# Kernel tuning notes

Measured on AMD Instinct MI355X. Metric: run time of the kernel, lower is better.

Reference implementation:

```python
import jax, jax.numpy as jnp
import numpy as np

N_NODES = 50000
N_EDGES = 800000
NUM_FEATURES = 128
HIDDEN = 128
EMBED = 64
OUT_DIM = 1


def setup_inputs() -> dict:
    key = jax.random.key(0)
    ks = jax.random.split(key, 12)
    x = jax.random.normal(ks[0], (N_NODES, NUM_FEATURES), dtype=jnp.float32)
    edge_index = jax.random.randint(ks[1], (2, N_EDGES), 0, N_NODES, dtype=jnp.int64)

    def glorot(k, fan_in, fan_out):
        s = jnp.sqrt(6.0 / (fan_in + fan_out)).astype(jnp.float32)
        return jax.random.uniform(k, (fan_in, fan_out), jnp.float32, -s, s)

    return {
        "x": x,
        "edge_index": edge_index,
        "W1": glorot(ks[2], NUM_FEATURES, HIDDEN),
        "b1": jnp.zeros((HIDDEN,), jnp.float32),
        "Wh": glorot(ks[3], HIDDEN, HIDDEN),
        "bh": jnp.zeros((HIDDEN,), jnp.float32),
        "W2": glorot(ks[4], HIDDEN, EMBED),
        "b2": jnp.zeros((EMBED,), jnp.float32),
        "Wout": glorot(ks[5], EMBED, OUT_DIM),
        "bout": jnp.zeros((OUT_DIM,), jnp.float32),
    }


def _gcn_norm(edge_index, num_nodes):
    # Add self-loops, compute symmetric normalization deg^{-1/2} A_hat deg^{-1/2}
    loop = jnp.arange(num_nodes, dtype=edge_index.dtype)
    src = jnp.concatenate([edge_index[0], loop])
    dst = jnp.concatenate([edge_index[1], loop])
    deg = jax.ops.segment_sum(jnp.ones_like(dst, dtype=jnp.float32), dst,
                              num_segments=num_nodes)
    dis = jnp.where(deg > 0, jax.lax.rsqrt(jnp.maximum(deg, 1.0)), 0.0)
    norm = dis[src] * dis[dst]  # [E+N]
    return src, dst, norm


def _gcn_conv(h, W, b, src, dst, norm, num_nodes):
    h = h @ W  # linear transform first (PyG GCNConv)
    msg = h[src] * norm[:, None]  # gather + scale
    return jax.ops.segment_sum(msg, dst, num_segments=num_nodes) + b


def reference(x, edge_index, W1, b1, Wh, bh, W2, b2, Wout, bout):
    n = x.shape[0]
    src, dst, norm = _gcn_norm(edge_index, n)
    h = jax.nn.relu(_gcn_conv(x, W1, b1, src, dst, norm, n))  # dropout p=0 -> identity
    h = jax.nn.relu(_gcn_conv(h, Wh, bh, src, dst, norm, n))
    h = _gcn_conv(h, W2, b2, src, dst, norm, n)
    out = h @ Wout + bout
    return (out, h)
```

## Files before the change

kernel.cpp:

```cpp
#include <hip/hip_runtime.h>
#include <hip/hip_bf16.h>


#define N_NODES 50000
#define N_EDGES 800000
#define NBUCK 196
#define GB 196
#define EPB 4096

typedef __attribute__((ext_vector_type(8))) short short8;
typedef __attribute__((ext_vector_type(8))) unsigned short ushort8v;
typedef __attribute__((ext_vector_type(4))) float f32x4;

static __device__ __forceinline__ unsigned short f2bf(float f) {
    __hip_bfloat16 h = __float2bfloat16(f);
    return *reinterpret_cast<unsigned short*>(&h);
}
static __device__ __forceinline__ float bf2f(unsigned short u) {
    return __uint_as_float(((unsigned)u) << 16);
}


__global__ __launch_bounds__(256) void hist_wprep_kernel(
    const int* __restrict__ dstv, int* __restrict__ H, int nE, int* __restrict__ ticket,
    const float* __restrict__ W1, const float* __restrict__ Wh, const float* __restrict__ W2,
    unsigned short* __restrict__ W1hi, unsigned short* __restrict__ W1lo,
    unsigned short* __restrict__ Whhi, unsigned short* __restrict__ Whlo,
    unsigned short* __restrict__ W2hi, unsigned short* __restrict__ W2lo) {
    int gt = blockIdx.x * 256 + threadIdx.x;
    if (gt == 0) *ticket = 0;
    if (gt < 40960) {
        const float* W;
        unsigned short *Hi, *Lo;
        int nout, lt;
        if (gt < 16384)      { W = W1; Hi = W1hi; Lo = W1lo; nout = 128; lt = gt; }
        else if (gt < 32768) { W = Wh; Hi = Whhi; Lo = Whlo; nout = 128; lt = gt - 16384; }
        else                 { W = W2; Hi = W2hi; Lo = W2lo; nout = 64;  lt = gt - 32768; }
        int col = lt % nout, k = lt / nout;
        float v = W[lt];
        unsigned short hi = f2bf(v);
        unsigned short lo = f2bf(v - bf2f(hi));
        Hi[(size_t)col * 128 + k] = hi;
        Lo[(size_t)col * 128 + k] = lo;
    }

    __shared__ int h[NBUCK];
    for (int i = threadIdx.x; i < NBUCK; i += 256) h[i] = 0;
    __syncthreads();
    int base = blockIdx.x * EPB;
#pragma unroll
    for (int i = 0; i < EPB / 256; ++i) {
        int e = base + i * 256 + threadIdx.x;
        if (e < nE) atomicAdd(&h[dstv[e] >> 8], 1);
    }
    __syncthreads();
    for (int i = threadIdx.x; i < NBUCK; i += 256)
        H[i * GB + blockIdx.x] = h[i];
}

__global__ __launch_bounds__(256) void scan_kernel(int* __restrict__ H,
                                                   int* __restrict__ bsum,
                                                   int* __restrict__ bstart,
                                                   int* __restrict__ rowoff_last,
                                                   int* __restrict__ ticket) {
    __shared__ int s[256];
    __shared__ int lastFlag;
    int t = threadIdx.x;
    int k = blockIdx.x;
    int v = (t < GB) ? H[k * GB + t] : 0;
    s[t] = v;
    __syncthreads();
    for (int off = 1; off < 256; off <<= 1) {
        int u = (t >= off) ? s[t - off] : 0;
        __syncthreads();
        s[t] += u;
        __syncthreads();
    }
    if (t < GB) H[k * GB + t] = s[t] - v;
    if (t == 255) {
        bsum[k] = s[255];
        __threadfence();
        int tk = atomicAdd(ticket, 1);
        lastFlag = (tk == NBUCK - 1);
    }
    __syncthreads();
    if (!lastFlag) return;
    __threadfence();
    int v2 = (t < NBUCK) ? bsum[t] : 0;
    s[t] = v2;
    __syncthreads();
    for (int off = 1; off < 256; off <<= 1) {
        int u = (t >= off) ? s[t - off] : 0;
        __syncthreads();
        s[t] += u;
        __syncthreads();
    }
    if (t < NBUCK) bstart[t] = s[t] - v2;
    if (t == 0) {
        bstart[NBUCK] = N_EDGES;
        *rowoff_last = N_EDGES;
    }
}

__global__ __launch_bounds__(256) void partition_kernel(const int* __restrict__ srcv,
                                                        const int* __restrict__ dstv,
                                                        const int* __restrict__ H,
                                                        const int* __restrict__ bstart,
                                                        unsigned int* __restrict__ P, int nE) {
    __shared__ int cur[NBUCK];
    for (int i = threadIdx.x; i < NBUCK; i += 256)
        cur[i] = bstart[i] + H[i * GB + blockIdx.x];
    __syncthreads();
    int base = blockIdx.x * EPB;
#pragma unroll
    for (int i = 0; i < EPB / 256; ++i) {
        int e = base + i * 256 + threadIdx.x;
        if (e < nE) {
            int d = dstv[e];
            unsigned int pk = (unsigned int)srcv[e] | ((unsigned int)(d & 255) << 16);
            int pos = atomicAdd(&cur[d >> 8], 1);
            P[pos] = pk;
        }
    }
}

__global__ __launch_bounds__(256) void bucket_csr_kernel(const unsigned int* __restrict__ P,
                                                         const int* __restrict__ bstart,
                                                         int* __restrict__ rowoff,
                                                         float* __restrict__ dis,
                                                         unsigned short* __restrict__ csr_src, int n) {
    __shared__ int cnt[256];
    __shared__ int s[256];
    __shared__ int cur[256];
    int t = threadIdx.x;
    int k = blockIdx.x;
    int ebeg = bstart[k], eend = bstart[k + 1];
    cnt[t] = 0;
    __syncthreads();
    for (int e = ebeg + t; e < eend; e += 256)
        atomicAdd(&cnt[(P[e] >> 16) & 255], 1);
    __syncthreads();
    int myc = cnt[t];
    s[t] = myc;
    __syncthreads();
    for (int off = 1; off < 256; off <<= 1) {
        int v = (t >= off) ? s[t - off] : 0;
        __syncthreads();
        s[t] += v;
        __syncthreads();
    }
    int excl = s[t] - myc;
    int node = (k << 8) + t;
    if (node < n) {
        rowoff[node] = ebeg + excl;
        dis[node] = rsqrtf((float)(myc + 1));
    }
    cur[t] = ebeg + excl;
    __syncthreads();
    for (int e = ebeg + t; e < eend; e += 256) {
        unsigned int p = P[e];
        int pos = atomicAdd(&cur[(p >> 16) & 255], 1);
        csr_src[pos] = (unsigned short)(p & 0xFFFFu);
    }
}

template <int NOUT, bool SPLITA>
__global__ __launch_bounds__(256) void gemm_mfma_kernel(
    const float* __restrict__ A,
    const unsigned short* __restrict__ Ahi,
    const unsigned short* __restrict__ Alo,
    const unsigned short* __restrict__ Wthi,
    const unsigned short* __restrict__ Wtlo,
    const float* __restrict__ scale,
    unsigned short* __restrict__ C, int M) {
    constexpr int LDK = 136;
    __shared__ unsigned short sAhi[64 * LDK];
    __shared__ unsigned short sAlo[64 * LDK];

    int tid = threadIdx.x;
    int w = tid >> 6, lane = tid & 63;
    int quad = lane >> 4, m = lane & 15;
    int Rbase = blockIdx.x * 64;
    int Cbase = blockIdx.y * 64;
    int r0 = (w & 1) * 32, c0 = (w >> 1) * 32;

    short8 bh[4][2], bl[4][2];
#pragma unroll
    for (int ks = 0; ks < 4; ++ks)
#pragma unroll
        for (int g = 0; g < 2; ++g) {
            size_t off = (size_t)(Cbase + c0 + g * 16 + m) * 128 + ks * 32 + quad * 8;
            bh[ks][g] = *(const short8*)(Wthi + off);
            bl[ks][g] = *(const short8*)(Wtlo + off);
        }

    if constexpr (SPLITA) {
        for (int i = tid; i < 64 * 16; i += 256) {
            int r = i >> 4, c8 = i & 15;
            int row = Rbase + r;
            short8 hv = {0, 0, 0, 0, 0, 0, 0, 0};
            short8 lv = {0, 0, 0, 0, 0, 0, 0, 0};
            if (row < M) {
                hv = *(const short8*)(Ahi + (size_t)row * 128 + c8 * 8);
                lv = *(const short8*)(Alo + (size_t)row * 128 + c8 * 8);
            }
            *(short8*)(sAhi + r * LDK + c8 * 8) = hv;
            *(short8*)(sAlo + r * LDK + c8 * 8) = lv;
        }
    } else {
        for (int i = tid; i < 64 * 32; i += 256) {
            int r = i >> 5, c4 = i & 31;
            int row = Rbase + r;
            float4 v = make_float4(0.f, 0.f, 0.f, 0.f);
            if (row < M) v = ((const float4*)(A + (size_t)row * 128))[c4];
            ushort4 hi, lo;
            hi.x = f2bf(v.x); lo.x = f2bf(v.x - bf2f(hi.x));
            hi.y = f2bf(v.y); lo.y = f2bf(v.y - bf2f(hi.y));
            hi.z = f2bf(v.z); lo.z = f2bf(v.z - bf2f(hi.z));
            hi.w = f2bf(v.w); lo.w = f2bf(v.w - bf2f(hi.w));
            *(ushort4*)(sAhi + r * LDK + c4 * 4) = hi;
            *(ushort4*)(sAlo + r * LDK + c4 * 4) = lo;
        }
    }
    __syncthreads();

    f32x4 z = {0.f, 0.f, 0.f, 0.f};
    f32x4 acc00 = z, acc01 = z, acc10 = z, acc11 = z;

#pragma unroll
    for (int ks = 0; ks < 4; ++ks) {
        int kof = ks * 32 + quad * 8;
        short8 ah0 = *(const short8*)(sAhi + (r0 + m) * LDK + kof);
        short8 ah1 = *(const short8*)(sAhi + (r0 + 16 + m) * LDK + kof);
        short8 al0 = *(const short8*)(sAlo + (r0 + m) * LDK + kof);
        short8 al1 = *(const short8*)(sAlo + (r0 + 16 + m) * LDK + kof);
        acc00 = __builtin_amdgcn_mfma_f32_16x16x32_bf16(ah0, bh[ks][0], acc00, 0, 0, 0);
        acc01 = __builtin_amdgcn_mfma_f32_16x16x32_bf16(ah0, bh[ks][1], acc01, 0, 0, 0);
        acc10 = __builtin_amdgcn_mfma_f32_16x16x32_bf16(ah1, bh[ks][0], acc10, 0, 0, 0);
        acc11 = __builtin_amdgcn_mfma_f32_16x16x32_bf16(ah1, bh[ks][1], acc11, 0, 0, 0);
        acc00 = __builtin_amdgcn_mfma_f32_16x16x32_bf16(ah0, bl[ks][0], acc00, 0, 0, 0);
        acc01 = __builtin_amdgcn_mfma_f32_16x16x32_bf16(ah0, bl[ks][1], acc01, 0, 0, 0);
        acc10 = __builtin_amdgcn_mfma_f32_16x16x32_bf16(ah1, bl[ks][0], acc10, 0, 0, 0);
        acc11 = __builtin_amdgcn_mfma_f32_16x16x32_bf16(ah1, bl[ks][1], acc11, 0, 0, 0);
        acc00 = __builtin_amdgcn_mfma_f32_16x16x32_bf16(al0, bh[ks][0], acc00, 0, 0, 0);
        acc01 = __builtin_amdgcn_mfma_f32_16x16x32_bf16(al0, bh[ks][1], acc01, 0, 0, 0);
        acc10 = __builtin_amdgcn_mfma_f32_16x16x32_bf16(al1, bh[ks][0], acc10, 0, 0, 0);
        acc11 = __builtin_amdgcn_mfma_f32_16x16x32_bf16(al1, bh[ks][1], acc11, 0, 0, 0);
    }

#pragma unroll
    for (int reg = 0; reg < 4; ++reg) {
        int row0g = Rbase + r0 + quad * 4 + reg;
        if (row0g < M) {
            float sc = scale[row0g];
            C[(size_t)row0g * NOUT + Cbase + c0 + m]      = f2bf(acc00[reg] * sc);
            C[(size_t)row0g * NOUT + Cbase + c0 + 16 + m] = f2bf(acc01[reg] * sc);
        }
        int row1g = row0g + 16;
        if (row1g < M) {
            float sc = scale[row1g];
            C[(size_t)row1g * NOUT + Cbase + c0 + m]      = f2bf(acc10[reg] * sc);
            C[(size_t)row1g * NOUT + Cbase + c0 + 16 + m] = f2bf(acc11[reg] * sc);
        }
    }
}

__global__ __launch_bounds__(256) void aggregate128_kernel(
    const int* __restrict__ rowoff, const unsigned short* __restrict__ csr_src,
    const float* __restrict__ dis, const unsigned short* __restrict__ tp,
    const float* __restrict__ bias,
    unsigned short* __restrict__ outHi, unsigned short* __restrict__ outLo, int n) {
    int wid = (blockIdx.x * 256 + threadIdx.x) >> 6;
    int lane = threadIdx.x & 63;
    int sub = lane >> 4, lc = lane & 15;
    int n0 = wid * 2;
    if (n0 >= n) return;
    int n1 = n0 + 1;
    bool has1 = (n1 < n);

    float a0[8] = {0.f, 0.f, 0.f, 0.f, 0.f, 0.f, 0.f, 0.f};
    float a1[8] = {0.f, 0.f, 0.f, 0.f, 0.f, 0.f, 0.f, 0.f};

#define ROW128(node) (*(const ushort8v*)(tp + (size_t)(node) * 128 + lc * 8))
#define ACC(a, u) { a[0] += bf2f(u[0]); a[1] += bf2f(u[1]); a[2] += bf2f(u[2]); a[3] += bf2f(u[3]); \
                    a[4] += bf2f(u[4]); a[5] += bf2f(u[5]); a[6] += bf2f(u[6]); a[7] += bf2f(u[7]); }

    if (sub == 0) { ushort8v u = ROW128(n0); ACC(a0, u); }
    else if (sub == 1 && has1) { ushort8v u = ROW128(n1); ACC(a1, u); }

    int mid = rowoff[n0 + 1];
    int i0 = rowoff[n0] + sub;
    int i1 = mid + sub;
    int end1 = has1 ? rowoff[n1 + 1] : mid;

    while (i0 + 12 < mid && i1 + 12 < end1) {
        int p0 = csr_src[i0], p1 = csr_src[i0 + 4], p2 = csr_src[i0 + 8], p3 = csr_src[i0 + 12];
        int q0 = csr_src[i1], q1 = csr_src[i1 + 4], q2 = csr_src[i1 + 8], q3 = csr_src[i1 + 12];
        ushort8v u0 = ROW128(p0), u1 = ROW128(p1), u2 = ROW128(p2), u3 = ROW128(p3);
        ushort8v v0 = ROW128(q0), v1 = ROW128(q1), v2 = ROW128(q2), v3 = ROW128(q3);
        ACC(a0, u0); ACC(a0, u1); ACC(a0, u2); ACC(a0, u3);
        ACC(a1, v0); ACC(a1, v1); ACC(a1, v2); ACC(a1, v3);
        i0 += 16; i1 += 16;
    }
    while (i0 + 4 < mid && i1 + 4 < end1) {
        int p0 = csr_src[i0], p1 = csr_src[i0 + 4];
        int q0 = csr_src[i1], q1 = csr_src[i1 + 4];
        ushort8v u0 = ROW128(p0), u1 = ROW128(p1);
        ushort8v v0 = ROW128(q0), v1 = ROW128(q1);
        ACC(a0, u0); ACC(a0, u1);
        ACC(a1, v0); ACC(a1, v1);
        i0 += 8; i1 += 8;
    }
    for (; i0 + 4 < mid; i0 += 8) {
        int p0 = csr_src[i0], p1 = csr_src[i0 + 4];
        ushort8v u0 = ROW128(p0), u1 = ROW128(p1);
        ACC(a0, u0); ACC(a0, u1);
    }
    for (; i0 < mid; i0 += 4) { ushort8v u = ROW128(csr_src[i0]); ACC(a0, u); }
    for (; i1 + 4 < end1; i1 += 8) {
        int q0 = csr_src[i1], q1 = csr_src[i1 + 4];
        ushort8v v0 = ROW128(q0), v1 = ROW128(q1);
        ACC(a1, v0); ACC(a1, v1);
    }
    for (; i1 < end1; i1 += 4) { ushort8v v = ROW128(csr_src[i1]); ACC(a1, v); }
#undef ROW128
#undef ACC

#pragma unroll
    for (int j = 0; j < 8; ++j) {
        a0[j] += __shfl_xor(a0[j], 16);
        a0[j] += __shfl_xor(a0[j], 32);
        a1[j] += __shfl_xor(a1[j], 16);
        a1[j] += __shfl_xor(a1[j], 32);
    }

    float* ap = (sub == 0) ? a0 : a1;
    int node = (sub == 0) ? n0 : n1;
    bool valid = (sub == 0) || (sub == 1 && has1);
    if (valid) {
        float dd = dis[node];
        float4 b0 = ((const float4*)bias)[lc * 2];
        float4 b1v = ((const float4*)bias)[lc * 2 + 1];
        float r[8];
        r[0] = fmaxf(ap[0] * dd + b0.x, 0.f);
        r[1] = fmaxf(ap[1] * dd + b0.y, 0.f);
        r[2] = fmaxf(ap[2] * dd + b0.z, 0.f);
        r[3] = fmaxf(ap[3] * dd + b0.w, 0.f);
        r[4] = fmaxf(ap[4] * dd + b1v.x, 0.f);
        r[5] = fmaxf(ap[5] * dd + b1v.y, 0.f);
        r[6] = fmaxf(ap[6] * dd + b1v.z, 0.f);
        r[7] = fmaxf(ap[7] * dd + b1v.w, 0.f);
        ushort8v hi, lo;
#pragma unroll
        for (int j = 0; j < 8; ++j) {
            hi[j] = f2bf(r[j]);
            lo[j] = f2bf(r[j] - bf2f(hi[j]));
        }
        *(ushort8v*)(outHi + (size_t)node * 128 + lc * 8) = hi;
        *(ushort8v*)(outLo + (size_t)node * 128 + lc * 8) = lo;
    }
}

__global__ __launch_bounds__(256) void aggregate64_head_kernel(
    const int* __restrict__ rowoff, const unsigned short* __restrict__ csr_src,
    const float* __restrict__ dis, const unsigned short* __restrict__ tp,
    const float* __restrict__ bias, const float* __restrict__ Wout,
    const float* __restrict__ bout, float* __restrict__ hout,
    float* __restrict__ out, int n) {
    int wid = (blockIdx.x * 256 + threadIdx.x) >> 6;
    int lane = threadIdx.x & 63;
    int sub = lane >> 4, lc = lane & 15;
    int n0 = wid * 2;
    if (n0 >= n) return;
    int n1 = n0 + 1;
    bool has1 = (n1 < n);

    float a0[4] = {0.f, 0.f, 0.f, 0.f};
    float a1[4] = {0.f, 0.f, 0.f, 0.f};

#define ROW64(node) (*((const ushort4*)(tp + (size_t)(node) * 64 + lc * 4)))
#define ACC2(a, u) { a[0] += bf2f(u.x); a[1] += bf2f(u.y); a[2] += bf2f(u.z); a[3] += bf2f(u.w); }

    if (sub == 0) { ushort4 u = ROW64(n0); ACC2(a0, u); }
    else if (sub == 1 && has1) { ushort4 u = ROW64(n1); ACC2(a1, u); }

    int mid = rowoff[n0 + 1];
    int i0 = rowoff[n0] + sub;
    int i1 = mid + sub;
    int end1 = has1 ? rowoff[n1 + 1] : mid;

    while (i0 + 12 < mid && i1 + 12 < end1) {
        int p0 = csr_src[i0], p1 = csr_src[i0 + 4], p2 = csr_src[i0 + 8], p3 = csr_src[i0 + 12];
        int q0 = csr_src[i1], q1 = csr_src[i1 + 4], q2 = csr_src[i1 + 8], q3 = csr_src[i1 + 12];
        ushort4 u0 = ROW64(p0), u1 = ROW64(p1), u2 = ROW64(p2), u3 = ROW64(p3);
        ushort4 v0 = ROW64(q0), v1 = ROW64(q1), v2 = ROW64(q2), v3 = ROW64(q3);
        ACC2(a0, u0); ACC2(a0, u1); ACC2(a0, u2); ACC2(a0, u3);
        ACC2(a1, v0); ACC2(a1, v1); ACC2(a1, v2); ACC2(a1, v3);
        i0 += 16; i1 += 16;
    }
    while (i0 + 4 < mid && i1 + 4 < end1) {
        int p0 = csr_src[i0], p1 = csr_src[i0 + 4];
        int q0 = csr_src[i1], q1 = csr_src[i1 + 4];
        ushort4 u0 = ROW64(p0), u1 = ROW64(p1);
        ushort4 v0 = ROW64(q0), v1 = ROW64(q1);
        ACC2(a0, u0); ACC2(a0, u1);
        ACC2(a1, v0); ACC2(a1, v1);
        i0 += 8; i1 += 8;
    }
    for (; i0 < mid; i0 += 4) { ushort4 u = ROW64(csr_src[i0]); ACC2(a0, u); }
    for (; i1 < end1; i1 += 4) { ushort4 v = ROW64(csr_src[i1]); ACC2(a1, v); }
#undef ROW64
#undef ACC2

#pragma unroll
    for (int j = 0; j < 4; ++j) {
        a0[j] += __shfl_xor(a0[j], 16);
        a0[j] += __shfl_xor(a0[j], 32);
        a1[j] += __shfl_xor(a1[j], 16);
        a1[j] += __shfl_xor(a1[j], 32);
    }

    float* ap = (sub == 0) ? a0 : a1;
    int node = (sub == 0) ? n0 : n1;
    bool valid = (sub == 0) || (sub == 1 && has1);
    float4 hv = make_float4(0.f, 0.f, 0.f, 0.f);
    if (valid) {
        float dd = dis[node];
        float4 b = ((const float4*)bias)[lc];
        hv.x = ap[0] * dd + b.x;
        hv.y = ap[1] * dd + b.y;
        hv.z = ap[2] * dd + b.z;
        hv.w = ap[3] * dd + b.w;
        ((float4*)(hout + (size_t)node * 64))[lc] = hv;
    }
    float4 wv = ((const float4*)Wout)[lc];
    float p = valid ? (hv.x * wv.x + hv.y * wv.y + hv.z * wv.z + hv.w * wv.w) : 0.f;
#pragma unroll
    for (int off = 8; off > 0; off >>= 1) p += __shfl_xor(p, off);
    if (lc == 0 && valid) out[node] = p + bout[0];
}

extern "C" void kernel_launch(void* const* d_in, const int* in_sizes, int n_in,
                              void* d_out, int out_size, void* d_ws, size_t ws_size,
                              hipStream_t stream) {
    const float* x    = (const float*)d_in[0];
    const int*   ei   = (const int*)d_in[1];
    const float* W1   = (const float*)d_in[2];
    const float* b1   = (const float*)d_in[3];
    const float* Wh   = (const float*)d_in[4];
    const float* bh   = (const float*)d_in[5];
    const float* W2   = (const float*)d_in[6];
    const float* b2   = (const float*)d_in[7];
    const float* Wout = (const float*)d_in[8];
    const float* bout = (const float*)d_in[9];

    const int N = N_NODES;
    const int E = N_EDGES;
    const int* srcv = ei;
    const int* dstv = ei + E;

    float* out  = (float*)d_out;
    float* hout = (float*)d_out + N;

    char* ws = (char*)d_ws;
    auto alloc = [&](size_t bytes) -> char* {
        char* p = ws;
        ws += (bytes + 255) & ~(size_t)255;
        return p;
    };
    int*   H       = (int*)alloc(sizeof(int) * NBUCK * GB);
    int*   bsum    = (int*)alloc(sizeof(int) * NBUCK);
    int*   bstart  = (int*)alloc(sizeof(int) * (NBUCK + 1));
    int*   ticket  = (int*)alloc(sizeof(int) * 4);
    int*   rowoff  = (int*)alloc(sizeof(int) * (N + 1));
    unsigned int* P = (unsigned int*)alloc(sizeof(unsigned int) * E);
    unsigned short* csr_src = (unsigned short*)alloc(sizeof(unsigned short) * (E + 2));
    float* dis     = (float*)alloc(sizeof(float) * N);
    unsigned short* W1thi = (unsigned short*)alloc(sizeof(unsigned short) * 128 * 128);
    unsigned short* W1tlo = (unsigned short*)alloc(sizeof(unsigned short) * 128 * 128);
    unsigned short* Whthi = (unsigned short*)alloc(sizeof(unsigned short) * 128 * 128);
    unsigned short* Whtlo = (unsigned short*)alloc(sizeof(unsigned short) * 128 * 128);
    unsigned short* W2thi = (unsigned short*)alloc(sizeof(unsigned short) * 64 * 128);
    unsigned short* W2tlo = (unsigned short*)alloc(sizeof(unsigned short) * 64 * 128);
    unsigned short* bufT  = (unsigned short*)alloc(sizeof(unsigned short) * (size_t)N * 128);
    unsigned short* bufHi = (unsigned short*)alloc(sizeof(unsigned short) * (size_t)N * 128);
    unsigned short* bufLo = (unsigned short*)alloc(sizeof(unsigned short) * (size_t)N * 128);

    hist_wprep_kernel<<<GB, 256, 0, stream>>>(dstv, H, E, ticket,
                                              W1, Wh, W2, W1thi, W1tlo, Whthi, Whtlo, W2thi, W2tlo);
    scan_kernel<<<NBUCK, 256, 0, stream>>>(H, bsum, bstart, rowoff + N, ticket);
    partition_kernel<<<GB, 256, 0, stream>>>(srcv, dstv, H, bstart, P, E);
    bucket_csr_kernel<<<NBUCK, 256, 0, stream>>>(P, bstart, rowoff, dis, csr_src, N);

    const int aggBlocks = ((N + 1) / 2 * 64 + 255) / 256;
    const int gemmRows = (N + 63) / 64;

    gemm_mfma_kernel<128, false><<<dim3(gemmRows, 2), 256, 0, stream>>>(
        x, nullptr, nullptr, W1thi, W1tlo, dis, bufT, N);
    aggregate128_kernel<<<aggBlocks, 256, 0, stream>>>(
        rowoff, csr_src, dis, bufT, b1, bufHi, bufLo, N);

    gemm_mfma_kernel<128, true><<<dim3(gemmRows, 2), 256, 0, stream>>>(
        nullptr, bufHi, bufLo, Whthi, Whtlo, dis, bufT, N);
    aggregate128_kernel<<<aggBlocks, 256, 0, stream>>>(
        rowoff, csr_src, dis, bufT, bh, bufHi, bufLo, N);

    gemm_mfma_kernel<64, true><<<dim3(gemmRows, 1), 256, 0, stream>>>(
        nullptr, bufHi, bufLo, W2thi, W2tlo, dis, bufT, N);
    aggregate64_head_kernel<<<aggBlocks, 256, 0, stream>>>(
        rowoff, csr_src, dis, bufT, b2, Wout, bout, hout, out, N);
}
```

Baseline: 277.9 us.

## Fuse first-layer GEMM with edge histogram and move source scaling into aggregation

The first GEMM (x@W1) no longer needs the degree scale, so it is merged into one launch with the edge histogram and the Wh/W2 weight prep, letting the graph-building work run concurrently with the GEMM. W1 prep moves to its own small kernel that runs first. Because layer-1 GEMM output is now unscaled, the first aggregation multiplies each gathered source row by dis[src]. That adds an extra scattered load per edge in that pass. It also adds one more launch and gives an unbalanced fused grid in exchange for overlap.

```diff
diff --git a/kernel.cpp b/kernel.cpp
--- a/kernel.cpp
+++ b/kernel.cpp
@@ -7,6 +7,8 @@
 #define NBUCK 196
 #define GB 196
 #define EPB 4096
+#define GEMM1ROWS ((N_NODES + 63) / 64)
+#define GEMM1B (GEMM1ROWS * 2)
 
 typedef __attribute__((ext_vector_type(8))) short short8;
 typedef __attribute__((ext_vector_type(8))) unsigned short ushort8v;
@@ -20,168 +22,17 @@
     return __uint_as_float(((unsigned)u) << 16);
 }
 
-
-__global__ __launch_bounds__(256) void hist_wprep_kernel(
-    const int* __restrict__ dstv, int* __restrict__ H, int nE, int* __restrict__ ticket,
-    const float* __restrict__ W1, const float* __restrict__ Wh, const float* __restrict__ W2,
-    unsigned short* __restrict__ W1hi, unsigned short* __restrict__ W1lo,
-    unsigned short* __restrict__ Whhi, unsigned short* __restrict__ Whlo,
-    unsigned short* __restrict__ W2hi, unsigned short* __restrict__ W2lo) {
-    int gt = blockIdx.x * 256 + threadIdx.x;
-    if (gt == 0) *ticket = 0;
-    if (gt < 40960) {
-        const float* W;
-        unsigned short *Hi, *Lo;
-        int nout, lt;
-        if (gt < 16384)      { W = W1; Hi = W1hi; Lo = W1lo; nout = 128; lt = gt; }
-        else if (gt < 32768) { W = Wh; Hi = Whhi; Lo = Whlo; nout = 128; lt = gt - 16384; }
-        else                 { W = W2; Hi = W2hi; Lo = W2lo; nout = 64;  lt = gt - 32768; }
-        int col = lt % nout, k = lt / nout;
-        float v = W[lt];
-        unsigned short hi = f2bf(v);
-        unsigned short lo = f2bf(v - bf2f(hi));
-        Hi[(size_t)col * 128 + k] = hi;
-        Lo[(size_t)col * 128 + k] = lo;
-    }
-
-    __shared__ int h[NBUCK];
-    for (int i = threadIdx.x; i < NBUCK; i += 256) h[i] = 0;
-    __syncthreads();
-    int base = blockIdx.x * EPB;
-#pragma unroll
-    for (int i = 0; i < EPB / 256; ++i) {
-        int e = base + i * 256 + threadIdx.x;
-        if (e < nE) atomicAdd(&h[dstv[e] >> 8], 1);
-    }
-    __syncthreads();
-    for (int i = threadIdx.x; i < NBUCK; i += 256)
-        H[i * GB + blockIdx.x] = h[i];
-}
-
-__global__ __launch_bounds__(256) void scan_kernel(int* __restrict__ H,
-                                                   int* __restrict__ bsum,
-                                                   int* __restrict__ bstart,
-                                                   int* __restrict__ rowoff_last,
-                                                   int* __restrict__ ticket) {
-    __shared__ int s[256];
-    __shared__ int lastFlag;
-    int t = threadIdx.x;
-    int k = blockIdx.x;
-    int v = (t < GB) ? H[k * GB + t] : 0;
-    s[t] = v;
-    __syncthreads();
-    for (int off = 1; off < 256; off <<= 1) {
-        int u = (t >= off) ? s[t - off] : 0;
-        __syncthreads();
-        s[t] += u;
-        __syncthreads();
-    }
-    if (t < GB) H[k * GB + t] = s[t] - v;
-    if (t == 255) {
-        bsum[k] = s[255];
-        __threadfence();
-        int tk = atomicAdd(ticket, 1);
-        lastFlag = (tk == NBUCK - 1);
-    }
-    __syncthreads();
-    if (!lastFlag) return;
-    __threadfence();
-    int v2 = (t < NBUCK) ? bsum[t] : 0;
-    s[t] = v2;
-    __syncthreads();
-    for (int off = 1; off < 256; off <<= 1) {
-        int u = (t >= off) ? s[t - off] : 0;
-        __syncthreads();
-        s[t] += u;
-        __syncthreads();
-    }
-    if (t < NBUCK) bstart[t] = s[t] - v2;
-    if (t == 0) {
-        bstart[NBUCK] = N_EDGES;
-        *rowoff_last = N_EDGES;
-    }
-}
-
-__global__ __launch_bounds__(256) void partition_kernel(const int* __restrict__ srcv,
-                                                        const int* __restrict__ dstv,
-                                                        const int* __restrict__ H,
-                                                        const int* __restrict__ bstart,
-                                                        unsigned int* __restrict__ P, int nE) {
-    __shared__ int cur[NBUCK];
-    for (int i = threadIdx.x; i < NBUCK; i += 256)
-        cur[i] = bstart[i] + H[i * GB + blockIdx.x];
-    __syncthreads();
-    int base = blockIdx.x * EPB;
-#pragma unroll
-    for (int i = 0; i < EPB / 256; ++i) {
-        int e = base + i * 256 + threadIdx.x;
-        if (e < nE) {
-            int d = dstv[e];
-            unsigned int pk = (unsigned int)srcv[e] | ((unsigned int)(d & 255) << 16);
-            int pos = atomicAdd(&cur[d >> 8], 1);
-            P[pos] = pk;
-        }
-    }
-}
-
-__global__ __launch_bounds__(256) void bucket_csr_kernel(const unsigned int* __restrict__ P,
-                                                         const int* __restrict__ bstart,
-                                                         int* __restrict__ rowoff,
-                                                         float* __restrict__ dis,
-                                                         unsigned short* __restrict__ csr_src, int n) {
-    __shared__ int cnt[256];
-    __shared__ int s[256];
-    __shared__ int cur[256];
-    int t = threadIdx.x;
-    int k = blockIdx.x;
-    int ebeg = bstart[k], eend = bstart[k + 1];
-    cnt[t] = 0;
-    __syncthreads();
-    for (int e = ebeg + t; e < eend; e += 256)
-        atomicAdd(&cnt[(P[e] >> 16) & 255], 1);
-    __syncthreads();
-    int myc = cnt[t];
-    s[t] = myc;
-    __syncthreads();
-    for (int off = 1; off < 256; off <<= 1) {
-        int v = (t >= off) ? s[t - off] : 0;
-        __syncthreads();
-        s[t] += v;
-        __syncthreads();
-    }
-    int excl = s[t] - myc;
-    int node = (k << 8) + t;
-    if (node < n) {
-        rowoff[node] = ebeg + excl;
-        dis[node] = rsqrtf((float)(myc + 1));
-    }
-    cur[t] = ebeg + excl;
-    __syncthreads();
-    for (int e = ebeg + t; e < eend; e += 256) {
-        unsigned int p = P[e];
-        int pos = atomicAdd(&cur[(p >> 16) & 255], 1);
-        csr_src[pos] = (unsigned short)(p & 0xFFFFu);
-    }
-}
-
-template <int NOUT, bool SPLITA>
-__global__ __launch_bounds__(256) void gemm_mfma_kernel(
+template <int NOUT, bool SPLITA, bool SCALED>
+static __device__ __forceinline__ void gemm_body(
+    unsigned short* sAhi, unsigned short* sAlo, int bx, int by, int tid,
     const float* __restrict__ A,
-    const unsigned short* __restrict__ Ahi,
-    const unsigned short* __restrict__ Alo,
-    const unsigned short* __restrict__ Wthi,
-    const unsigned short* __restrict__ Wtlo,
-    const float* __restrict__ scale,
-    unsigned short* __restrict__ C, int M) {
+    const unsigned short* __restrict__ Ahi, const unsigned short* __restrict__ Alo,
+    const unsigned short* __restrict__ Wthi, const unsigned short* __restrict__ Wtlo,
+    const float* __restrict__ scale, unsigned short* __restrict__ C, int M) {
     constexpr int LDK = 136;
-    __shared__ unsigned short sAhi[64 * LDK];
-    __shared__ unsigned short sAlo[64 * LDK];
-
-    int tid = threadIdx.x;
     int w = tid >> 6, lane = tid & 63;
     int quad = lane >> 4, m = lane & 15;
-    int Rbase = blockIdx.x * 64;
-    int Cbase = blockIdx.y * 64;
+    int Rbase = bx * 64, Cbase = by * 64;
     int r0 = (w & 1) * 32, c0 = (w >> 1) * 32;
 
     short8 bh[4][2], bl[4][2];
@@ -198,8 +49,7 @@
         for (int i = tid; i < 64 * 16; i += 256) {
             int r = i >> 4, c8 = i & 15;
             int row = Rbase + r;
-            short8 hv = {0, 0, 0, 0, 0, 0, 0, 0};
-            short8 lv = {0, 0, 0, 0, 0, 0, 0, 0};
+            short8 hv = {0,0,0,0,0,0,0,0}, lv = {0,0,0,0,0,0,0,0};
             if (row < M) {
                 hv = *(const short8*)(Ahi + (size_t)row * 128 + c8 * 8);
                 lv = *(const short8*)(Alo + (size_t)row * 128 + c8 * 8);
@@ -252,19 +102,194 @@
     for (int reg = 0; reg < 4; ++reg) {
         int row0g = Rbase + r0 + quad * 4 + reg;
         if (row0g < M) {
-            float sc = scale[row0g];
+            float sc = SCALED ? scale[row0g] : 1.0f;
             C[(size_t)row0g * NOUT + Cbase + c0 + m]      = f2bf(acc00[reg] * sc);
             C[(size_t)row0g * NOUT + Cbase + c0 + 16 + m] = f2bf(acc01[reg] * sc);
         }
         int row1g = row0g + 16;
         if (row1g < M) {
-            float sc = scale[row1g];
+            float sc = SCALED ? scale[row1g] : 1.0f;
             C[(size_t)row1g * NOUT + Cbase + c0 + m]      = f2bf(acc10[reg] * sc);
             C[(size_t)row1g * NOUT + Cbase + c0 + 16 + m] = f2bf(acc11[reg] * sc);
         }
     }
 }
 
+__global__ __launch_bounds__(256) void w1prep_kernel(
+    const float* __restrict__ W1,
+    unsigned short* __restrict__ Hi, unsigned short* __restrict__ Lo) {
+    int gt = blockIdx.x * 256 + threadIdx.x;
+    int col = gt & 127, k = gt >> 7;
+    float v = W1[gt];
+    unsigned short hi = f2bf(v);
+    unsigned short lo = f2bf(v - bf2f(hi));
+    Hi[(size_t)col * 128 + k] = hi;
+    Lo[(size_t)col * 128 + k] = lo;
+}
+
+__global__ __launch_bounds__(256) void fat_gemm1_hist_kernel(
+    const float* __restrict__ x,
+    const unsigned short* __restrict__ W1thi, const unsigned short* __restrict__ W1tlo,
+    unsigned short* __restrict__ C,
+    const int* __restrict__ dstv, int* __restrict__ H, int nE, int* __restrict__ ticket,
+    const float* __restrict__ Wh, const float* __restrict__ W2,
+    unsigned short* __restrict__ Whhi, unsigned short* __restrict__ Whlo,
+    unsigned short* __restrict__ W2hi, unsigned short* __restrict__ W2lo) {
+    constexpr int LDK = 136;
+    __shared__ unsigned short sAhi[64 * LDK];
+    __shared__ unsigned short sAlo[64 * LDK];
+
+    int gb = blockIdx.x;
+    if (gb < GEMM1B) {
+        gemm_body<128, false, false>(sAhi, sAlo, gb >> 1, gb & 1, threadIdx.x,
+                                     x, nullptr, nullptr, W1thi, W1tlo, nullptr, C, N_NODES);
+        return;
+    }
+    int hb = gb - GEMM1B;
+
+    if (hb == 0 && threadIdx.x == 0) *ticket = 0;
+    int gt = hb * 256 + threadIdx.x;
+    if (gt < 24576) {
+        const float* W; unsigned short *Hi, *Lo; int nout, lt;
+        if (gt < 16384) { W = Wh; Hi = Whhi; Lo = Whlo; nout = 128; lt = gt; }
+        else            { W = W2; Hi = W2hi; Lo = W2lo; nout = 64;  lt = gt - 16384; }
+        int col = lt % nout, k = lt / nout;
+        float v = W[lt];
+        unsigned short hi = f2bf(v);
+        unsigned short lo = f2bf(v - bf2f(hi));
+        Hi[(size_t)col * 128 + k] = hi;
+        Lo[(size_t)col * 128 + k] = lo;
+    }
+
+    int* h = (int*)sAhi;
+    for (int i = threadIdx.x; i < NBUCK; i += 256) h[i] = 0;
+    __syncthreads();
+    int base = hb * EPB;
+#pragma unroll
+    for (int i = 0; i < EPB / 256; ++i) {
+        int e = base + i * 256 + threadIdx.x;
+        if (e < nE) atomicAdd(&h[dstv[e] >> 8], 1);
+    }
+    __syncthreads();
+    for (int i = threadIdx.x; i < NBUCK; i += 256)
+        H[i * GB + hb] = h[i];
+}
+
+__global__ __launch_bounds__(256) void scan_kernel(int* __restrict__ H,
+                                                   int* __restrict__ bsum,
+                                                   int* __restrict__ bstart,
+                                                   int* __restrict__ rowoff_last,
+                                                   int* __restrict__ ticket) {
+    __shared__ int s[256];
+    __shared__ int lastFlag;
+    int t = threadIdx.x, k = blockIdx.x;
+    int v = (t < GB) ? H[k * GB + t] : 0;
+    s[t] = v;
+    __syncthreads();
+    for (int off = 1; off < 256; off <<= 1) {
+        int u = (t >= off) ? s[t - off] : 0;
+        __syncthreads();
+        s[t] += u;
+        __syncthreads();
+    }
+    if (t < GB) H[k * GB + t] = s[t] - v;
+    if (t == 255) {
+        bsum[k] = s[255];
+        __threadfence();
+        int tk = atomicAdd(ticket, 1);
+        lastFlag = (tk == NBUCK - 1);
+    }
+    __syncthreads();
+    if (!lastFlag) return;
+    __threadfence();
+    int v2 = (t < NBUCK) ? bsum[t] : 0;
+    s[t] = v2;
+    __syncthreads();
+    for (int off = 1; off < 256; off <<= 1) {
+        int u = (t >= off) ? s[t - off] : 0;
+        __syncthreads();
+        s[t] += u;
+        __syncthreads();
+    }
+    if (t < NBUCK) bstart[t] = s[t] - v2;
+    if (t == 0) { bstart[NBUCK] = N_EDGES; *rowoff_last = N_EDGES; }
+}
+
+__global__ __launch_bounds__(256) void partition_kernel(const int* __restrict__ srcv,
+                                                        const int* __restrict__ dstv,
+                                                        const int* __restrict__ H,
+                                                        const int* __restrict__ bstart,
+                                                        unsigned int* __restrict__ P, int nE) {
+    __shared__ int cur[NBUCK];
+    for (int i = threadIdx.x; i < NBUCK; i += 256)
+        cur[i] = bstart[i] + H[i * GB + blockIdx.x];
+    __syncthreads();
+    int base = blockIdx.x * EPB;
+#pragma unroll
+    for (int i = 0; i < EPB / 256; ++i) {
+        int e = base + i * 256 + threadIdx.x;
+        if (e < nE) {
+            int d = dstv[e];
+            unsigned int pk = (unsigned int)srcv[e] | ((unsigned int)(d & 255) << 16);
+            int pos = atomicAdd(&cur[d >> 8], 1);
+            P[pos] = pk;
+        }
+    }
+}
+
+__global__ __launch_bounds__(256) void bucket_csr_kernel(const unsigned int* __restrict__ P,
+                                                         const int* __restrict__ bstart,
+                                                         int* __restrict__ rowoff,
+                                                         float* __restrict__ dis,
+                                                         unsigned short* __restrict__ csr_src, int n) {
+    __shared__ int cnt[256];
+    __shared__ int s[256];
+    __shared__ int cur[256];
+    int t = threadIdx.x, k = blockIdx.x;
+    int ebeg = bstart[k], eend = bstart[k + 1];
+    cnt[t] = 0;
+    __syncthreads();
+    for (int e = ebeg + t; e < eend; e += 256)
+        atomicAdd(&cnt[(P[e] >> 16) & 255], 1);
+    __syncthreads();
+    int myc = cnt[t];
+    s[t] = myc;
+    __syncthreads();
+    for (int off = 1; off < 256; off <<= 1) {
+        int v = (t >= off) ? s[t - off] : 0;
+        __syncthreads();
+        s[t] += v;
+        __syncthreads();
+    }
+    int excl = s[t] - myc;
+    int node = (k << 8) + t;
+    if (node < n) {
+        rowoff[node] = ebeg + excl;
+        dis[node] = rsqrtf((float)(myc + 1));
+    }
+    cur[t] = ebeg + excl;
+    __syncthreads();
+    for (int e = ebeg + t; e < eend; e += 256) {
+        unsigned int p = P[e];
+        int pos = atomicAdd(&cur[(p >> 16) & 255], 1);
+        csr_src[pos] = (unsigned short)(p & 0xFFFFu);
+    }
+}
+
+template <int NOUT, bool SPLITA>
+__global__ __launch_bounds__(256) void gemm_mfma_kernel(
+    const float* __restrict__ A,
+    const unsigned short* __restrict__ Ahi, const unsigned short* __restrict__ Alo,
+    const unsigned short* __restrict__ Wthi, const unsigned short* __restrict__ Wtlo,
+    const float* __restrict__ scale, unsigned short* __restrict__ C, int M) {
+    constexpr int LDK = 136;
+    __shared__ unsigned short sAhi[64 * LDK];
+    __shared__ unsigned short sAlo[64 * LDK];
+    gemm_body<NOUT, SPLITA, true>(sAhi, sAlo, blockIdx.x, blockIdx.y, threadIdx.x,
+                                  A, Ahi, Alo, Wthi, Wtlo, scale, C, M);
+}
+
+template <bool SRCSCALE>
 __global__ __launch_bounds__(256) void aggregate128_kernel(
     const int* __restrict__ rowoff, const unsigned short* __restrict__ csr_src,
     const float* __restrict__ dis, const unsigned short* __restrict__ tp,
@@ -278,15 +303,18 @@
     int n1 = n0 + 1;
     bool has1 = (n1 < n);
 
-    float a0[8] = {0.f, 0.f, 0.f, 0.f, 0.f, 0.f, 0.f, 0.f};
-    float a1[8] = {0.f, 0.f, 0.f, 0.f, 0.f, 0.f, 0.f, 0.f};
+    float a0[8] = {0.f,0.f,0.f,0.f,0.f,0.f,0.f,0.f};
+    float a1[8] = {0.f,0.f,0.f,0.f,0.f,0.f,0.f,0.f};
 
 #define ROW128(node) (*(const ushort8v*)(tp + (size_t)(node) * 128 + lc * 8))
-#define ACC(a, u) { a[0] += bf2f(u[0]); a[1] += bf2f(u[1]); a[2] += bf2f(u[2]); a[3] += bf2f(u[3]); \
-                    a[4] += bf2f(u[4]); a[5] += bf2f(u[5]); a[6] += bf2f(u[6]); a[7] += bf2f(u[7]); }
-
-    if (sub == 0) { ushort8v u = ROW128(n0); ACC(a0, u); }
-    else if (sub == 1 && has1) { ushort8v u = ROW128(n1); ACC(a1, u); }
+#define ACCS(a, u, s) { a[0] += bf2f(u[0]) * s; a[1] += bf2f(u[1]) * s; \
+                        a[2] += bf2f(u[2]) * s; a[3] += bf2f(u[3]) * s; \
+                        a[4] += bf2f(u[4]) * s; a[5] += bf2f(u[5]) * s; \
+                        a[6] += bf2f(u[6]) * s; a[7] += bf2f(u[7]) * s; }
+#define SC(node) (SRCSCALE ? dis[node] : 1.0f)
+
+    if (sub == 0) { float s = SC(n0); ushort8v u = ROW128(n0); ACCS(a0, u, s); }
+    else if (sub == 1 && has1) { float s = SC(n1); ushort8v u = ROW128(n1); ACCS(a1, u, s); }
 
     int mid = rowoff[n0 + 1];
     int i0 = rowoff[n0] + sub;
@@ -296,35 +324,41 @@
     while (i0 + 12 < mid && i1 + 12 < end1) {
         int p0 = csr_src[i0], p1 = csr_src[i0 + 4], p2 = csr_src[i0 + 8], p3 = csr_src[i0 + 12];
         int q0 = csr_src[i1], q1 = csr_src[i1 + 4], q2 = csr_src[i1 + 8], q3 = csr_src[i1 + 12];
+        float sp0 = SC(p0), sp1 = SC(p1), sp2 = SC(p2), sp3 = SC(p3);
+        float sq0 = SC(q0), sq1 = SC(q1), sq2 = SC(q2), sq3 = SC(q3);
         ushort8v u0 = ROW128(p0), u1 = ROW128(p1), u2 = ROW128(p2), u3 = ROW128(p3);
         ushort8v v0 = ROW128(q0), v1 = ROW128(q1), v2 = ROW128(q2), v3 = ROW128(q3);
-        ACC(a0, u0); ACC(a0, u1); ACC(a0, u2); ACC(a0, u3);
-        ACC(a1, v0); ACC(a1, v1); ACC(a1, v2); ACC(a1, v3);
+        ACCS(a0, u0, sp0); ACCS(a0, u1, sp1); ACCS(a0, u2, sp2); ACCS(a0, u3, sp3);
+        ACCS(a1, v0, sq0); ACCS(a1, v1, sq1); ACCS(a1, v2, sq2); ACCS(a1, v3, sq3);
         i0 += 16; i1 += 16;
     }
     while (i0 + 4 < mid && i1 + 4 < end1) {
         int p0 = csr_src[i0], p1 = csr_src[i0 + 4];
         int q0 = csr_src[i1], q1 = csr_src[i1 + 4];
+        float sp0 = SC(p0), sp1 = SC(p1), sq0 = SC(q0), sq1 = SC(q1);
         ushort8v u0 = ROW128(p0), u1 = ROW128(p1);
         ushort8v v0 = ROW128(q0), v1 = ROW128(q1);
-        ACC(a0, u0); ACC(a0, u1);
-        ACC(a1, v0); ACC(a1, v1);
+        ACCS(a0, u0, sp0); ACCS(a0, u1, sp1);
+        ACCS(a1, v0, sq0); ACCS(a1, v1, sq1);
         i0 += 8; i1 += 8;
     }
     for (; i0 + 4 < mid; i0 += 8) {
         int p0 = csr_src[i0], p1 = csr_src[i0 + 4];
+        float sp0 = SC(p0), sp1 = SC(p1);
         ushort8v u0 = ROW128(p0), u1 = ROW128(p1);
-        ACC(a0, u0); ACC(a0, u1);
-    }
-    for (; i0 < mid; i0 += 4) { ushort8v u = ROW128(csr_src[i0]); ACC(a0, u); }
+        ACCS(a0, u0, sp0); ACCS(a0, u1, sp1);
+    }
+    for (; i0 < mid; i0 += 4) { int p = csr_src[i0]; float s = SC(p); ushort8v u = ROW128(p); ACCS(a0, u, s); }
     for (; i1 + 4 < end1; i1 += 8) {
         int q0 = csr_src[i1], q1 = csr_src[i1 + 4];
+        float sq0 = SC(q0), sq1 = SC(q1);
         ushort8v v0 = ROW128(q0), v1 = ROW128(q1);
-        ACC(a1, v0); ACC(a1, v1);
-    }
-    for (; i1 < end1; i1 += 4) { ushort8v v = ROW128(csr_src[i1]); ACC(a1, v); }
+        ACCS(a1, v0, sq0); ACCS(a1, v1, sq1);
+    }
+    for (; i1 < end1; i1 += 4) { int q = csr_src[i1]; float s = SC(q); ushort8v v = ROW128(q); ACCS(a1, v, s); }
 #undef ROW128
-#undef ACC
+#undef ACCS
+#undef SC
 
 #pragma unroll
     for (int j = 0; j < 8; ++j) {
@@ -375,8 +409,8 @@
     int n1 = n0 + 1;
     bool has1 = (n1 < n);
 
-    float a0[4] = {0.f, 0.f, 0.f, 0.f};
-    float a1[4] = {0.f, 0.f, 0.f, 0.f};
+    float a0[4] = {0.f,0.f,0.f,0.f};
+    float a1[4] = {0.f,0.f,0.f,0.f};
 
 #define ROW64(node) (*((const ushort4*)(tp + (size_t)(node) * 64 + lc * 4)))
 #define ACC2(a, u) { a[0] += bf2f(u.x); a[1] += bf2f(u.y); a[2] += bf2f(u.z); a[3] += bf2f(u.w); }
@@ -486,8 +520,13 @@
     unsigned short* bufHi = (unsigned short*)alloc(sizeof(unsigned short) * (size_t)N * 128);
     unsigned short* bufLo = (unsigned short*)alloc(sizeof(unsigned short) * (size_t)N * 128);
 
-    hist_wprep_kernel<<<GB, 256, 0, stream>>>(dstv, H, E, ticket,
-                                              W1, Wh, W2, W1thi, W1tlo, Whthi, Whtlo, W2thi, W2tlo);
+    w1prep_kernel<<<64, 256, 0, stream>>>(W1, W1thi, W1tlo);
+
+    fat_gemm1_hist_kernel<<<GEMM1B + GB, 256, 0, stream>>>(
+        x, W1thi, W1tlo, bufT,
+        dstv, H, E, ticket,
+        Wh, W2, Whthi, Whtlo, W2thi, W2tlo);
+
     scan_kernel<<<NBUCK, 256, 0, stream>>>(H, bsum, bstart, rowoff + N, ticket);
     partition_kernel<<<GB, 256, 0, stream>>>(srcv, dstv, H, bstart, P, E);
     bucket_csr_kernel<<<NBUCK, 256, 0, stream>>>(P, bstart, rowoff, dis, csr_src, N);
@@ -495,14 +534,12 @@
     const int aggBlocks = ((N + 1) / 2 * 64 + 255) / 256;
     const int gemmRows = (N + 63) / 64;
 
-    gemm_mfma_kernel<128, false><<<dim3(gemmRows, 2), 256, 0, stream>>>(
-        x, nullptr, nullptr, W1thi, W1tlo, dis, bufT, N);
-    aggregate128_kernel<<<aggBlocks, 256, 0, stream>>>(
+    aggregate128_kernel<true><<<aggBlocks, 256, 0, stream>>>(
         rowoff, csr_src, dis, bufT, b1, bufHi, bufLo, N);
 
     gemm_mfma_kernel<128, true><<<dim3(gemmRows, 2), 256, 0, stream>>>(
         nullptr, bufHi, bufLo, Whthi, Whtlo, dis, bufT, N);
-    aggregate128_kernel<<<aggBlocks, 256, 0, stream>>>(
+    aggregate128_kernel<false><<<aggBlocks, 256, 0, stream>>>(
         rowoff, csr_src, dis, bufT, bh, bufHi, bufLo, N);
 
     gemm_mfma_kernel<64, true><<<dim3(gemmRows, 1), 256, 0, stream>>>(
```

Result: no change. 283.0 us (+1.8%).
